# Kernel tuning notes

Measured on AMD Instinct MI355X. Metric: run time of the kernel, lower is better.

The kernel has to match this reference:

```python
import jax, jax.numpy as jnp
import numpy as np

N = 4096   # num_nodes
W = 12     # window_size
H = 256    # hidden_dim
P = 10     # prediction_horizon
E = 131072 # num edges (avg degree 32)


def setup_inputs() -> dict:
    key = jax.random.key(0)
    ks = jax.random.split(key, 12)
    return {
        "x": jax.random.normal(ks[0], (N, W), jnp.float32),
        "edge_index": jax.random.randint(ks[1], (2, E), 0, N, jnp.int32),
        "edge_weight": jax.random.uniform(ks[2], (E,), jnp.float32),
        "gcn_w": jax.random.normal(ks[3], (H,), jnp.float32) * 0.2,
        "ta_w": jax.random.normal(ks[4], (W * H, H), jnp.float32) * 0.02,
        "ta_b": jnp.zeros((H,), jnp.float32),
        "w_ih": jax.random.normal(ks[5], (3 * H, H), jnp.float32) * 0.05,
        "w_hh": jax.random.normal(ks[6], (3 * H, H), jnp.float32) * 0.05,
        "b_ih": jnp.zeros((3 * H,), jnp.float32),
        "b_hh": jnp.zeros((3 * H,), jnp.float32),
        "out_w": jax.random.normal(ks[7], (H,), jnp.float32) * 0.05,
        "out_b": jnp.zeros((1,), jnp.float32),
    }


def _laplacian(edge_index, edge_weight):
    # dense adjacency with self loops, symmetric normalization D^-1/2 (A+I)^T D^-1/2
    adj = jnp.zeros((N, N), edge_weight.dtype).at[edge_index[0], edge_index[1]].set(edge_weight)
    adj = adj + jnp.eye(N, dtype=edge_weight.dtype)
    d = jnp.power(adj.sum(1), -0.5)
    d = jnp.where(jnp.isinf(d), 0.0, d)
    # torch: adj.matmul(diag(d)).T.matmul(diag(d)) == ((adj * d[None,:]).T) * d[None,:]
    return (adj * d[None, :]).T * d[None, :]


def _gru_cell(x, h, w_ih, w_hh, b_ih, b_hh):
    gx = x @ w_ih.T + b_ih          # (N, 3H)
    gh = h @ w_hh.T + b_hh          # (N, 3H)
    xr, xz, xn = jnp.split(gx, 3, axis=-1)
    hr, hz, hn = jnp.split(gh, 3, axis=-1)
    r = jax.nn.sigmoid(xr + hr)
    z = jax.nn.sigmoid(xz + hz)
    n = jnp.tanh(xn + r * hn)
    return (1.0 - z) * n + z * h


def reference(x, edge_index, edge_weight, gcn_w, ta_w, ta_b,
              w_ih, w_hh, b_ih, b_hh, out_w, out_b):
    L = _laplacian(edge_index, edge_weight)  # fixed across all horizon steps

    def single_step(window, h):
        ax = L @ window                                   # (N, W)
        # outer product with weight vector + tanh, flattened per node
        g = jnp.tanh(ax[:, :, None] * gcn_w[None, None, :]).reshape(N, W * H)
        t = jax.nn.relu(g @ ta_w + ta_b)                  # (N, H)
        h2 = _gru_cell(t, h, w_ih, w_hh, b_ih, b_hh)      # (N, H)
        pred = h2 @ out_w + out_b[0]                      # (N,)
        return pred, h2

    def scan_step(carry, _):
        window, h = carry
        pred, h2 = single_step(window, h)
        new_window = jnp.concatenate(
            [window[:, 1:], jax.lax.stop_gradient(pred)[:, None]], axis=1)
        return (new_window, h2), pred

    h0 = jnp.zeros((N, H), x.dtype)
    _, preds = jax.lax.scan(scan_step, (x, h0), None, length=P)  # (P, N)
    return preds.T  # (N, P)
```

## Files before the change

### kernel.cpp

```cpp
#include <hip/hip_runtime.h>
#include <math.h>

#define NN 4096
#define WW 12
#define HH 256
#define PP 10
#define EE 131072
#define HS 262144
#define HMASK (HS-1)
#define TS 192
#define TA 8.0f
#define RS 22

typedef __attribute__((ext_vector_type(8))) _Float16 half8v;
typedef __attribute__((ext_vector_type(4))) _Float16 half4v;
typedef __attribute__((ext_vector_type(4))) float f32x4;

__device__ __forceinline__ float fast_tanh(float x){
  float e = __expf(2.0f*x);
  return 1.0f - 2.0f/(e+1.0f);
}
__device__ __forceinline__ float fast_sigmoid(float x){
  return 1.0f/(1.0f+__expf(-x));
}


__global__ void k_init(const float* __restrict__ x, int* keys, int* midx,
                       float* deg, int* cnt, float* ring, float* hA, int* count){
  int i = blockIdx.x*256 + threadIdx.x;
  if (i < HS){ keys[i] = -1; midx[i] = -1; }
  if (i < NN){ deg[i] = 0.0f; cnt[i] = 0; }
  if (i < NN*WW){ int n = i/WW, w = i - n*WW; ring[n*RS + w] = x[i]; }
  if (i < NN*HH) hA[i] = 0.0f;
  if (i == 0) *count = 0;
}

__global__ void k_insert(const int* __restrict__ ei, int* keys, int* midx){
  int e = blockIdx.x*256 + threadIdx.x;
  if (e >= EE) return;
  int key = ei[e]*NN + ei[EE+e];
  unsigned h = (((unsigned)key)*2654435761u >> 14) & HMASK;
  for(;;){
    int k = keys[h];
    if (k == key){ atomicMax(&midx[h], e); return; }
    if (k == -1){
      int old = atomicCAS(&keys[h], -1, key);
      if (old == -1 || old == key){ atomicMax(&midx[h], e); return; }
    }
    h = (h+1) & HMASK;
  }
}

__global__ void k_compact(const int* __restrict__ ei, const float* __restrict__ ew,
                          const int* __restrict__ keys, const int* __restrict__ midx,
                          int* wsrc, int* wdst, float* wwt,
                          float* deg, int* cnt, int* count){
  int e = blockIdx.x*256 + threadIdx.x;
  if (e >= EE) return;
  int src = ei[e], dst = ei[EE+e];
  int key = src*NN + dst;
  unsigned h = (((unsigned)key)*2654435761u >> 14) & HMASK;
  while (keys[h] != key) h = (h+1) & HMASK;
  if (midx[h] == e){
    int p = atomicAdd(count, 1);
    wsrc[p] = src; wdst[p] = dst; wwt[p] = ew[e];
    atomicAdd(&deg[src], ew[e]);
    atomicAdd(&cnt[dst], 1);
  }
}

__global__ __launch_bounds__(1024) void k_scan(const int* __restrict__ cnt,
                                               int* row_start, int* fill){
  __shared__ int sd[NN];
  int tid = threadIdx.x;
  for (int i = tid; i < NN; i += 1024) sd[i] = cnt[i];
  __syncthreads();
  for (int off = 1; off < NN; off <<= 1){
    int v[4];
    #pragma unroll
    for (int r = 0; r < 4; ++r){
      int i = tid + r*1024;
      v[r] = (i >= off) ? sd[i-off] : 0;
    }
    __syncthreads();
    #pragma unroll
    for (int r = 0; r < 4; ++r) sd[tid + r*1024] += v[r];
    __syncthreads();
  }
  for (int i = tid; i < NN; i += 1024){
    int incl = sd[i];
    row_start[i+1] = incl;
    fill[i] = incl - cnt[i];
  }
  if (tid == 0) row_start[0] = 0;
}

__global__ void k_scatter(const int* __restrict__ wsrc, const int* __restrict__ wdst,
                          const float* __restrict__ wwt, const float* __restrict__ deg,
                          int* fill, int* csr_src, float* csr_cf,
                          const int* __restrict__ count){
  int p = blockIdx.x*256 + threadIdx.x;
  if (p >= *count) return;
  int s = wsrc[p], d = wdst[p];
  float c = wwt[p] * (1.0f/sqrtf(deg[s]+1.0f)) * (1.0f/sqrtf(deg[d]+1.0f));
  int pos = atomicAdd(&fill[d], 1);
  csr_src[pos] = s;
  csr_cf[pos] = c;
}

__global__ __launch_bounds__(256) void k_tab(const float* __restrict__ gcn_w,
                                             const float* __restrict__ ta_w,
                                             float* __restrict__ tab){
  __shared__ float As[32][64];
  __shared__ float Bs[32][64];
  __shared__ float gws[256];
  int tid = threadIdx.x;
  int n0 = blockIdx.x*64;
  int m0 = blockIdx.y*64;
  int w  = blockIdx.z;
  gws[tid] = gcn_w[tid];
  __syncthreads();
  float acc[4][4] = {};
  int tm = tid >> 4, tn = tid & 15;
  const float astep = 2.0f*TA/TS;
  for (int k0 = 0; k0 < 256; k0 += 32){
    #pragma unroll
    for (int r = 0; r < 2; ++r){
      int f = tid + r*256;
      int kk = f >> 4, n4 = (f & 15)*4;
      *(float4*)&Bs[kk][n4] = *(const float4*)&ta_w[(w*256 + k0+kk)*HH + n0 + n4];
    }
    {
      int kk = tid >> 3;
      int mb = (tid & 7)*8;
      float gw = gws[k0 + kk];
      #pragma unroll
      for (int i2 = 0; i2 < 8; ++i2){
        float a = -TA + (float)(m0 + mb + i2)*astep;
        As[kk][mb+i2] = fast_tanh(a*gw);
      }
    }
    __syncthreads();
    #pragma unroll
    for (int kk = 0; kk < 32; ++kk){
      float4 a4 = *(float4*)&As[kk][tm*4];
      float4 b4 = *(float4*)&Bs[kk][tn*4];
      float a[4] = {a4.x,a4.y,a4.z,a4.w};
      float b[4] = {b4.x,b4.y,b4.z,b4.w};
      #pragma unroll
      for (int i = 0; i < 4; ++i)
        #pragma unroll
        for (int j = 0; j < 4; ++j)
          acc[i][j] = fmaf(a[i], b[j], acc[i][j]);
    }
    __syncthreads();
  }
  #pragma unroll
  for (int i = 0; i < 4; ++i){
    int row = m0 + tm*4 + i;
    if (row <= TS){
      #pragma unroll
      for (int j = 0; j < 4; ++j)
        tab[((size_t)w*(TS+1) + row)*HH + n0 + tn*4 + j] = acc[i][j];
    }
  }
}

__global__ void k_wpack(const float* __restrict__ w_ih, const float* __restrict__ w_hh,
                        _Float16* __restrict__ wp){
  int idx = blockIdx.x*256 + threadIdx.x;
  int lane = idx & 63;
  int rest = idx >> 6;
  int ct = rest & 15; rest >>= 4;
  int g  = rest & 3;
  int ks = rest >> 2;
  int col = ct*16 + (lane & 15);
  int kb  = ks*32 + (lane >> 4)*8;
  _Float16 w8[8];
  #pragma unroll
  for (int j = 0; j < 8; ++j){
    int k = kb + j;
    float v;
    if      (g == 0) v = (k < 256) ? w_ih[col*HH + k]        : w_hh[col*HH + k - 256];
    else if (g == 1) v = (k < 256) ? w_ih[(256+col)*HH + k]  : w_hh[(256+col)*HH + k - 256];
    else if (g == 2) v = (k < 256) ? w_ih[(512+col)*HH + k]  : 0.0f;
    else             v = (k < 256) ? 0.0f                    : w_hh[(512+col)*HH + k - 256];
    w8[j] = (_Float16)v;
  }
  *(half8v*)&wp[(size_t)idx*8] = *(half8v*)w8;
}

__global__ __launch_bounds__(1024, 4) void k_step(
    const int* __restrict__ rowst, const int* __restrict__ csr_src,
    const float* __restrict__ csr_cf, const float* __restrict__ deg,
    float* __restrict__ ring, const float* __restrict__ tab,
    const float* __restrict__ ta_b,
    const float* __restrict__ hc, float* __restrict__ hnb,
    const _Float16* __restrict__ wp,
    const float* __restrict__ b_ih, const float* __restrict__ b_hh,
    const float* __restrict__ out_w, const float* __restrict__ out_b,
    float* __restrict__ out, int s){

  __shared__ __align__(16) _Float16 Xh[64][17][8];
  __shared__ __align__(16) _Float16 Xl[64][17][8];
  __shared__ __align__(16) float h_pad[16][260];
  __shared__ int   sidx[16][12];
  __shared__ float sfrac[16][12];

  const int tid = threadIdx.x;
  const int n0 = blockIdx.x*16;
  const int wv = tid >> 6, lane = tid & 63;

  {
    int row = tid >> 6;
    int c0 = (tid & 63)*4;
    float4 v = *(const float4*)(hc + (size_t)(n0+row)*HH + c0);
    *(float4*)&h_pad[row][c0] = v;
    float f[4] = {v.x,v.y,v.z,v.w};
    _Float16 h4[4], l4[4];
    #pragma unroll
    for (int j = 0; j < 4; ++j){
      h4[j] = (_Float16)f[j];
      l4[j] = (_Float16)(f[j] - (float)h4[j]);
    }
    int koct = 32 + (c0 >> 3), elem = c0 & 7;
    *(half4v*)&Xh[koct][row][elem] = *(half4v*)h4;
    *(half4v*)&Xl[koct][row][elem] = *(half4v*)l4;
  }
  if (lane < 48){
    int w = lane >> 2, g = lane & 3;
    int node = n0 + wv;
    float acc0 = 0.0f;
    if (g == 0){
      float dv2 = 1.0f/(deg[node] + 1.0f);
      acc0 = dv2*ring[(size_t)node*RS + s + w];
    }
    int e1 = rowst[node+1];
    for (int e = rowst[node] + g; e < e1; e += 4)
      acc0 += csr_cf[e]*ring[(size_t)csr_src[e]*RS + s + w];
    acc0 += __shfl_xor(acc0, 1, 64);
    acc0 += __shfl_xor(acc0, 2, 64);
    if (g == 0){
      float u = (acc0 + TA) * ((float)TS/(2.0f*TA));
      u = fminf(fmaxf(u, 0.0f), (float)TS - 0.0005f);
      int i = (int)u;
      sidx[wv][w] = i;
      sfrac[wv][w] = u - (float)i;
    }
  }
  __syncthreads();

  {
    int col = tid & 255;
    int r0 = (tid >> 8)*4;
    int koct = col >> 3, elem = col & 7;
    float tb = ta_b[col];
    #pragma unroll
    for (int rr = 0; rr < 4; ++rr){
      int r = r0 + rr;
      float acc0 = tb;
      #pragma unroll
      for (int w = 0; w < 12; ++w){
        const float* pj = tab + ((size_t)w*(TS+1) + sidx[r][w])*HH + col;
        float v0 = pj[0], v1 = pj[HH];
        acc0 += v0 + sfrac[r][w]*(v1 - v0);
      }
      float tv = acc0 > 0.0f ? acc0 : 0.0f;
      _Float16 hh_ = (_Float16)tv;
      Xh[koct][r][elem] = hh_;
      Xl[koct][r][elem] = (_Float16)(tv - (float)hh_);
    }
  }
  __syncthreads();

  f32x4 acc[4];
  #pragma unroll
  for (int g = 0; g < 4; ++g) acc[g] = (f32x4){0.f,0.f,0.f,0.f};

  const int a_row = lane & 15, a_ko = lane >> 4;
  const size_t fbase = (size_t)wv*64 + lane;

  half8v b0[2], b1[2], b2[2];

#define LOADB(KS, BUF)                                                        \
  {                                                                           \
    const int G2v = ((KS) < 8) ? 2 : 3;                                       \
    const size_t fb = fbase + (size_t)(KS)*4096;                              \
    b0[BUF] = *(const half8v*)&wp[fb*8];                                      \
    b1[BUF] = *(const half8v*)&wp[(fb + 1024)*8];                             \
    b2[BUF] = *(const half8v*)&wp[(fb + (size_t)G2v*1024)*8];                 \
  }

  LOADB(0, 0)
  #pragma unroll
  for (int ks = 0; ks < 16; ++ks){
    const int cur = ks & 1, nxt = cur ^ 1;
    if (ks < 15) LOADB(ks+1, nxt)
    half8v ah = *(const half8v*)&Xh[ks*4 + a_ko][a_row][0];
    half8v al = *(const half8v*)&Xl[ks*4 + a_ko][a_row][0];
    const int G2 = (ks < 8) ? 2 : 3;
    acc[0]  = __builtin_amdgcn_mfma_f32_16x16x32_f16(ah, b0[cur], acc[0], 0,0,0);
    acc[0]  = __builtin_amdgcn_mfma_f32_16x16x32_f16(al, b0[cur], acc[0], 0,0,0);
    acc[1]  = __builtin_amdgcn_mfma_f32_16x16x32_f16(ah, b1[cur], acc[1], 0,0,0);
    acc[1]  = __builtin_amdgcn_mfma_f32_16x16x32_f16(al, b1[cur], acc[1], 0,0,0);
    acc[G2] = __builtin_amdgcn_mfma_f32_16x16x32_f16(ah, b2[cur], acc[G2], 0,0,0);
    acc[G2] = __builtin_amdgcn_mfma_f32_16x16x32_f16(al, b2[cur], acc[G2], 0,0,0);
  }
#undef LOADB
  __syncthreads();

  {
    const int ecl  = lane & 15;
    const int erow = (lane >> 4)*4;
    const int col  = wv*16 + ecl;
    float br  = b_ih[col]        + b_hh[col];
    float bz  = b_ih[col + HH]   + b_hh[col + HH];
    float bxn = b_ih[col + 2*HH];
    float bhn = b_hh[col + 2*HH];
    #pragma unroll
    for (int q = 0; q < 4; ++q){
      int row = erow + q;
      float r = fast_sigmoid(acc[0][q] + br);
      float z = fast_sigmoid(acc[1][q] + bz);
      float n = fast_tanh(acc[2][q] + bxn + r*(acc[3][q] + bhn));
      float hv = h_pad[row][col];
      float hp = (1.0f - z)*n + z*hv;
      hnb[(size_t)(n0+row)*HH + col] = hp;
      h_pad[row][col] = hp;
    }
  }
  __syncthreads();

  {
    int c0 = lane*4;
    float4 hv = *(const float4*)&h_pad[wv][c0];
    float4 w4 = *(const float4*)(out_w + c0);
    float sacc = hv.x*w4.x + hv.y*w4.y + hv.z*w4.z + hv.w*w4.w;
    sacc += __shfl_xor(sacc, 1, 64);
    sacc += __shfl_xor(sacc, 2, 64);
    sacc += __shfl_xor(sacc, 4, 64);
    sacc += __shfl_xor(sacc, 8, 64);
    sacc += __shfl_xor(sacc, 16, 64);
    sacc += __shfl_xor(sacc, 32, 64);
    if (lane == 0){
      float pv = sacc + out_b[0];
      out[(size_t)(n0+wv)*PP + s] = pv;
      ring[(size_t)(n0+wv)*RS + 12 + s] = pv;
    }
  }
}


extern "C" void kernel_launch(void* const* d_in, const int* in_sizes, int n_in,
                              void* d_out, int out_size, void* d_ws, size_t ws_size,
                              hipStream_t stream){
  const float* x     = (const float*)d_in[0];
  const int*   ei    = (const int*)  d_in[1];
  const float* ew    = (const float*)d_in[2];
  const float* gcn_w = (const float*)d_in[3];
  const float* ta_w  = (const float*)d_in[4];
  const float* ta_b  = (const float*)d_in[5];
  const float* w_ih  = (const float*)d_in[6];
  const float* w_hh  = (const float*)d_in[7];
  const float* b_ih  = (const float*)d_in[8];
  const float* b_hh  = (const float*)d_in[9];
  const float* out_w = (const float*)d_in[10];
  const float* out_b = (const float*)d_in[11];
  float* out = (float*)d_out;

  char* p = (char*)d_ws;
  float*    tab     = (float*)p;    p += (size_t)12*(TS+1)*HH*4;
  int*      keys    = (int*)p;      p += (size_t)HS*4;
  int*      midx    = (int*)p;      p += (size_t)HS*4;
  int*      wsrc    = (int*)p;      p += (size_t)EE*4;
  int*      wdst    = (int*)p;      p += (size_t)EE*4;
  float*    wwt     = (float*)p;    p += (size_t)EE*4;
  int*      csr_src = (int*)p;      p += (size_t)EE*4;
  float*    csr_cf  = (float*)p;    p += (size_t)EE*4;
  float*    deg     = (float*)p;    p += (size_t)NN*4;
  int*      cnt     = (int*)p;      p += (size_t)NN*4;
  int*      fill    = (int*)p;      p += (size_t)NN*4;
  int*      rowst   = (int*)p;      p += (size_t)(NN+64)*4;
  int*      count   = (int*)p;      p += 256;
  float*    ring    = (float*)p;    p += (size_t)NN*RS*4;
  float*    hA      = (float*)p;    p += (size_t)NN*HH*4;
  float*    hB      = (float*)p;    p += (size_t)NN*HH*4;
  _Float16* wp      = (_Float16*)p; p += (size_t)16*4*16*64*8*2;

  k_init   <<<(NN*HH)/256, 256, 0, stream>>>(x, keys, midx, deg, cnt, ring, hA, count);
  k_insert <<<EE/256, 256, 0, stream>>>(ei, keys, midx);
  k_compact<<<EE/256, 256, 0, stream>>>(ei, ew, keys, midx, wsrc, wdst, wwt, deg, cnt, count);
  k_scan   <<<1, 1024, 0, stream>>>(cnt, rowst, fill);
  k_scatter<<<EE/256, 256, 0, stream>>>(wsrc, wdst, wwt, deg, fill, csr_src, csr_cf, count);
  k_wpack  <<<256, 256, 0, stream>>>(w_ih, w_hh, wp);
  k_tab    <<<dim3(HH/64, (TS+64)/64, WW), 256, 0, stream>>>(gcn_w, ta_w, tab);

  for (int s = 0; s < PP; ++s){
    const float* hc  = (s & 1) ? hB : hA;
    float*       hnb = (s & 1) ? hA : hB;
    k_step<<<NN/16, 1024, 0, stream>>>(rowst, csr_src, csr_cf, deg, ring, tab,
                                       ta_b, hc, hnb, wp,
                                       b_ih, b_hh, out_w, out_b, out, s);
  }
}
```

Baseline: 296.2 us.

## Retile GRU step to 32 nodes x 128 columns with split-K and fp16 table

Measured after the change: 354.3 us. +19.6%, slower.

```diff
diff --git a/kernel.cpp b/kernel.cpp
--- a/kernel.cpp
+++ b/kernel.cpp
@@ -13,7 +13,6 @@
 #define RS 22
 
 typedef __attribute__((ext_vector_type(8))) _Float16 half8v;
-typedef __attribute__((ext_vector_type(4))) _Float16 half4v;
 typedef __attribute__((ext_vector_type(4))) float f32x4;
 
 __device__ __forceinline__ float fast_tanh(float x){
@@ -26,11 +25,13 @@
 
 
 __global__ void k_init(const float* __restrict__ x, int* keys, int* midx,
-                       float* deg, int* cnt, float* ring, float* hA, int* count){
+                       float* deg, int* cnt, float* ring, float* hA,
+                       float* out, int* count){
   int i = blockIdx.x*256 + threadIdx.x;
   if (i < HS){ keys[i] = -1; midx[i] = -1; }
   if (i < NN){ deg[i] = 0.0f; cnt[i] = 0; }
   if (i < NN*WW){ int n = i/WW, w = i - n*WW; ring[n*RS + w] = x[i]; }
+  if (i < NN*PP){ int n = i/PP, c = i - n*PP; ring[n*RS + 12 + c] = 0.0f; out[i] = 0.0f; }
   if (i < NN*HH) hA[i] = 0.0f;
   if (i == 0) *count = 0;
 }
@@ -110,7 +111,7 @@
 
 __global__ __launch_bounds__(256) void k_tab(const float* __restrict__ gcn_w,
                                              const float* __restrict__ ta_w,
-                                             float* __restrict__ tab){
+                                             _Float16* __restrict__ tab16){
   __shared__ float As[32][64];
   __shared__ float Bs[32][64];
   __shared__ float gws[256];
@@ -161,7 +162,7 @@
     if (row <= TS){
       #pragma unroll
       for (int j = 0; j < 4; ++j)
-        tab[((size_t)w*(TS+1) + row)*HH + n0 + tn*4 + j] = acc[i][j];
+        tab16[((size_t)w*(TS+1) + row)*HH + n0 + tn*4 + j] = (_Float16)acc[i][j];
     }
   }
 }
@@ -190,10 +191,10 @@
   *(half8v*)&wp[(size_t)idx*8] = *(half8v*)w8;
 }
 
-__global__ __launch_bounds__(1024, 4) void k_step(
+__global__ __launch_bounds__(1024) void k_step(
     const int* __restrict__ rowst, const int* __restrict__ csr_src,
     const float* __restrict__ csr_cf, const float* __restrict__ deg,
-    float* __restrict__ ring, const float* __restrict__ tab,
+    float* __restrict__ ring, const _Float16* __restrict__ tab16,
     const float* __restrict__ ta_b,
     const float* __restrict__ hc, float* __restrict__ hnb,
     const _Float16* __restrict__ wp,
@@ -201,68 +202,78 @@
     const float* __restrict__ out_w, const float* __restrict__ out_b,
     float* __restrict__ out, int s){
 
-  __shared__ __align__(16) _Float16 Xh[64][17][8];
-  __shared__ __align__(16) _Float16 Xl[64][17][8];
-  __shared__ __align__(16) float h_pad[16][260];
-  __shared__ int   sidx[16][12];
-  __shared__ float sfrac[16][12];
+  __shared__ __align__(16) _Float16 Xh[64][33][8];
+  __shared__ __align__(16) _Float16 Xl[64][33][8];
+  __shared__ __align__(16) float h_pad[32][132];
+  __shared__ float pex[8][2][64][13];
+  __shared__ int   sidx[32][12];
+  __shared__ float sfrac[32][12];
 
   const int tid = threadIdx.x;
-  const int n0 = blockIdx.x*16;
+  const int bx = blockIdx.x;
+  const int n0 = (bx >> 1)*32;
+  const int ch = bx & 1;
+  const int c0g = ch*128;
   const int wv = tid >> 6, lane = tid & 63;
+  const int ct = wv & 7, kh = wv >> 3;
 
   {
-    int row = tid >> 6;
-    int c0 = (tid & 63)*4;
-    float4 v = *(const float4*)(hc + (size_t)(n0+row)*HH + c0);
-    *(float4*)&h_pad[row][c0] = v;
-    float f[4] = {v.x,v.y,v.z,v.w};
-    _Float16 h4[4], l4[4];
-    #pragma unroll
-    for (int j = 0; j < 4; ++j){
-      h4[j] = (_Float16)f[j];
-      l4[j] = (_Float16)(f[j] - (float)h4[j]);
-    }
-    int koct = 32 + (c0 >> 3), elem = c0 & 7;
-    *(half4v*)&Xh[koct][row][elem] = *(half4v*)h4;
-    *(half4v*)&Xl[koct][row][elem] = *(half4v*)l4;
+    int row = tid >> 5;
+    int c = (tid & 31)*8;
+    const float* hr = hc + (size_t)(n0+row)*HH + c;
+    float4 v0 = *(const float4*)hr, v1 = *(const float4*)(hr+4);
+    float f[8] = {v0.x,v0.y,v0.z,v0.w,v1.x,v1.y,v1.z,v1.w};
+    _Float16 h8[8], l8[8];
+    #pragma unroll
+    for (int j = 0; j < 8; ++j){
+      h8[j] = (_Float16)f[j];
+      l8[j] = (_Float16)(f[j] - (float)h8[j]);
+    }
+    int koct = 32 + (c >> 3);
+    *(half8v*)&Xh[koct][row][0] = *(half8v*)h8;
+    *(half8v*)&Xl[koct][row][0] = *(half8v*)l8;
+    if ((c >> 7) == ch){
+      *(float4*)&h_pad[row][c & 127]       = v0;
+      *(float4*)&h_pad[row][(c & 127) + 4] = v1;
+    }
   }
   if (lane < 48){
-    int w = lane >> 2, g = lane & 3;
-    int node = n0 + wv;
+    int nl = lane/24;
+    int rem = lane - nl*24;
+    int w = rem >> 1, g = rem & 1;
+    int node = n0 + wv*2 + nl;
     float acc0 = 0.0f;
     if (g == 0){
       float dv2 = 1.0f/(deg[node] + 1.0f);
       acc0 = dv2*ring[(size_t)node*RS + s + w];
     }
     int e1 = rowst[node+1];
-    for (int e = rowst[node] + g; e < e1; e += 4)
+    for (int e = rowst[node] + g; e < e1; e += 2)
       acc0 += csr_cf[e]*ring[(size_t)csr_src[e]*RS + s + w];
     acc0 += __shfl_xor(acc0, 1, 64);
-    acc0 += __shfl_xor(acc0, 2, 64);
     if (g == 0){
       float u = (acc0 + TA) * ((float)TS/(2.0f*TA));
       u = fminf(fmaxf(u, 0.0f), (float)TS - 0.0005f);
       int i = (int)u;
-      sidx[wv][w] = i;
-      sfrac[wv][w] = u - (float)i;
+      sidx[wv*2+nl][w] = i;
+      sfrac[wv*2+nl][w] = u - (float)i;
     }
   }
   __syncthreads();
 
   {
     int col = tid & 255;
-    int r0 = (tid >> 8)*4;
+    int r0 = (tid >> 8)*8;
     int koct = col >> 3, elem = col & 7;
     float tb = ta_b[col];
     #pragma unroll
-    for (int rr = 0; rr < 4; ++rr){
+    for (int rr = 0; rr < 8; ++rr){
       int r = r0 + rr;
       float acc0 = tb;
       #pragma unroll
       for (int w = 0; w < 12; ++w){
-        const float* pj = tab + ((size_t)w*(TS+1) + sidx[r][w])*HH + col;
-        float v0 = pj[0], v1 = pj[HH];
+        const _Float16* pj = tab16 + ((size_t)w*(TS+1) + sidx[r][w])*HH + col;
+        float v0 = (float)pj[0], v1 = (float)pj[HH];
         acc0 += v0 + sfrac[r][w]*(v1 - v0);
       }
       float tv = acc0 > 0.0f ? acc0 : 0.0f;
@@ -273,79 +284,107 @@
   }
   __syncthreads();
 
-  f32x4 acc[4];
+  f32x4 acc[3][2];
   #pragma unroll
-  for (int g = 0; g < 4; ++g) acc[g] = (f32x4){0.f,0.f,0.f,0.f};
-
+  for (int g = 0; g < 3; ++g){
+    acc[g][0] = (f32x4){0.f,0.f,0.f,0.f};
+    acc[g][1] = (f32x4){0.f,0.f,0.f,0.f};
+  }
   const int a_row = lane & 15, a_ko = lane >> 4;
-  const size_t fbase = (size_t)wv*64 + lane;
-
+  const int ctg = ch*8 + ct;
+  const size_t goff2 = (size_t)(kh ? 3 : 2)*1024;
+  const size_t fb0 = (size_t)ctg*64 + lane;
   half8v b0[2], b1[2], b2[2];
 
-#define LOADB(KS, BUF)                                                        \
+#define LOADB(K8, BUF)                                                        \
   {                                                                           \
-    const int G2v = ((KS) < 8) ? 2 : 3;                                       \
-    const size_t fb = fbase + (size_t)(KS)*4096;                              \
+    const size_t fb = fb0 + (size_t)(kh*8 + (K8))*4096;                       \
     b0[BUF] = *(const half8v*)&wp[fb*8];                                      \
     b1[BUF] = *(const half8v*)&wp[(fb + 1024)*8];                             \
-    b2[BUF] = *(const half8v*)&wp[(fb + (size_t)G2v*1024)*8];                 \
+    b2[BUF] = *(const half8v*)&wp[(fb + goff2)*8];                            \
   }
 
   LOADB(0, 0)
   #pragma unroll
-  for (int ks = 0; ks < 16; ++ks){
-    const int cur = ks & 1, nxt = cur ^ 1;
-    if (ks < 15) LOADB(ks+1, nxt)
-    half8v ah = *(const half8v*)&Xh[ks*4 + a_ko][a_row][0];
-    half8v al = *(const half8v*)&Xl[ks*4 + a_ko][a_row][0];
-    const int G2 = (ks < 8) ? 2 : 3;
-    acc[0]  = __builtin_amdgcn_mfma_f32_16x16x32_f16(ah, b0[cur], acc[0], 0,0,0);
-    acc[0]  = __builtin_amdgcn_mfma_f32_16x16x32_f16(al, b0[cur], acc[0], 0,0,0);
-    acc[1]  = __builtin_amdgcn_mfma_f32_16x16x32_f16(ah, b1[cur], acc[1], 0,0,0);
-    acc[1]  = __builtin_amdgcn_mfma_f32_16x16x32_f16(al, b1[cur], acc[1], 0,0,0);
-    acc[G2] = __builtin_amdgcn_mfma_f32_16x16x32_f16(ah, b2[cur], acc[G2], 0,0,0);
-    acc[G2] = __builtin_amdgcn_mfma_f32_16x16x32_f16(al, b2[cur], acc[G2], 0,0,0);
+  for (int k8 = 0; k8 < 8; ++k8){
+    const int cur = k8 & 1, nxt = cur ^ 1;
+    if (k8 < 7) LOADB(k8+1, nxt)
+    int ko = (kh*8 + k8)*4 + a_ko;
+    half8v ah0 = *(const half8v*)&Xh[ko][a_row][0];
+    half8v al0 = *(const half8v*)&Xl[ko][a_row][0];
+    half8v ah1 = *(const half8v*)&Xh[ko][16 + a_row][0];
+    half8v al1 = *(const half8v*)&Xl[ko][16 + a_row][0];
+    acc[0][0] = __builtin_amdgcn_mfma_f32_16x16x32_f16(ah0, b0[cur], acc[0][0], 0,0,0);
+    acc[0][0] = __builtin_amdgcn_mfma_f32_16x16x32_f16(al0, b0[cur], acc[0][0], 0,0,0);
+    acc[0][1] = __builtin_amdgcn_mfma_f32_16x16x32_f16(ah1, b0[cur], acc[0][1], 0,0,0);
+    acc[0][1] = __builtin_amdgcn_mfma_f32_16x16x32_f16(al1, b0[cur], acc[0][1], 0,0,0);
+    acc[1][0] = __builtin_amdgcn_mfma_f32_16x16x32_f16(ah0, b1[cur], acc[1][0], 0,0,0);
+    acc[1][0] = __builtin_amdgcn_mfma_f32_16x16x32_f16(al0, b1[cur], acc[1][0], 0,0,0);
+    acc[1][1] = __builtin_amdgcn_mfma_f32_16x16x32_f16(ah1, b1[cur], acc[1][1], 0,0,0);
+    acc[1][1] = __builtin_amdgcn_mfma_f32_16x16x32_f16(al1, b1[cur], acc[1][1], 0,0,0);
+    acc[2][0] = __builtin_amdgcn_mfma_f32_16x16x32_f16(ah0, b2[cur], acc[2][0], 0,0,0);
+    acc[2][0] = __builtin_amdgcn_mfma_f32_16x16x32_f16(al0, b2[cur], acc[2][0], 0,0,0);
+    acc[2][1] = __builtin_amdgcn_mfma_f32_16x16x32_f16(ah1, b2[cur], acc[2][1], 0,0,0);
+    acc[2][1] = __builtin_amdgcn_mfma_f32_16x16x32_f16(al1, b2[cur], acc[2][1], 0,0,0);
   }
 #undef LOADB
   __syncthreads();
 
-  {
-    const int ecl  = lane & 15;
-    const int erow = (lane >> 4)*4;
-    const int col  = wv*16 + ecl;
+  if (kh == 0){
+    #pragma unroll
+    for (int rf = 0; rf < 2; ++rf)
+      #pragma unroll
+      for (int g3 = 0; g3 < 3; ++g3)
+        #pragma unroll
+        for (int q = 0; q < 4; ++q)
+          pex[ct][rf][lane][g3*4 + q] = acc[g3][rf][q];
+  }
+  __syncthreads();
+
+  if (kh == 1){
+    const int ecl = lane & 15;
+    const int col_l = ct*16 + ecl;
+    const int col = c0g + col_l;
     float br  = b_ih[col]        + b_hh[col];
     float bz  = b_ih[col + HH]   + b_hh[col + HH];
     float bxn = b_ih[col + 2*HH];
     float bhn = b_hh[col + 2*HH];
     #pragma unroll
-    for (int q = 0; q < 4; ++q){
-      int row = erow + q;
-      float r = fast_sigmoid(acc[0][q] + br);
-      float z = fast_sigmoid(acc[1][q] + bz);
-      float n = fast_tanh(acc[2][q] + bxn + r*(acc[3][q] + bhn));
-      float hv = h_pad[row][col];
-      float hp = (1.0f - z)*n + z*hv;
-      hnb[(size_t)(n0+row)*HH + col] = hp;
-      h_pad[row][col] = hp;
+    for (int rf = 0; rf < 2; ++rf){
+      #pragma unroll
+      for (int q = 0; q < 4; ++q){
+        int row = rf*16 + (lane >> 4)*4 + q;
+        float xr = pex[ct][rf][lane][q]     + acc[0][rf][q];
+        float xz = pex[ct][rf][lane][4 + q] + acc[1][rf][q];
+        float xn = pex[ct][rf][lane][8 + q];
+        float hn = acc[2][rf][q];
+        float r = fast_sigmoid(xr + br);
+        float z = fast_sigmoid(xz + bz);
+        float n = fast_tanh(xn + bxn + r*(hn + bhn));
+        float hv = h_pad[row][col_l];
+        float hp = (1.0f - z)*n + z*hv;
+        hnb[(size_t)(n0+row)*HH + col] = hp;
+        h_pad[row][col_l] = hp;
+      }
     }
   }
   __syncthreads();
 
   {
-    int c0 = lane*4;
-    float4 hv = *(const float4*)&h_pad[wv][c0];
-    float4 w4 = *(const float4*)(out_w + c0);
+    int row = 2*wv + (lane >> 5);
+    int cl = (lane & 31)*4;
+    float4 hv = *(const float4*)&h_pad[row][cl];
+    float4 w4 = *(const float4*)(out_w + c0g + cl);
     float sacc = hv.x*w4.x + hv.y*w4.y + hv.z*w4.z + hv.w*w4.w;
     sacc += __shfl_xor(sacc, 1, 64);
     sacc += __shfl_xor(sacc, 2, 64);
     sacc += __shfl_xor(sacc, 4, 64);
     sacc += __shfl_xor(sacc, 8, 64);
     sacc += __shfl_xor(sacc, 16, 64);
-    sacc += __shfl_xor(sacc, 32, 64);
-    if (lane == 0){
-      float pv = sacc + out_b[0];
-      out[(size_t)(n0+wv)*PP + s] = pv;
-      ring[(size_t)(n0+wv)*RS + 12 + s] = pv;
+    if ((lane & 31) == 0){
+      float part = sacc + (ch == 0 ? out_b[0] : 0.0f);
+      atomicAdd(&out[(size_t)(n0+row)*PP + s], part);
+      atomicAdd(&ring[(size_t)(n0+row)*RS + 12 + s], part);
     }
   }
 }
@@ -369,7 +408,7 @@
   float* out = (float*)d_out;
 
   char* p = (char*)d_ws;
-  float*    tab     = (float*)p;    p += (size_t)12*(TS+1)*HH*4;
+  _Float16* tab16   = (_Float16*)p; p += (size_t)12*(TS+1)*HH*2;
   int*      keys    = (int*)p;      p += (size_t)HS*4;
   int*      midx    = (int*)p;      p += (size_t)HS*4;
   int*      wsrc    = (int*)p;      p += (size_t)EE*4;
@@ -387,18 +426,18 @@
   float*    hB      = (float*)p;    p += (size_t)NN*HH*4;
   _Float16* wp      = (_Float16*)p; p += (size_t)16*4*16*64*8*2;
 
-  k_init   <<<(NN*HH)/256, 256, 0, stream>>>(x, keys, midx, deg, cnt, ring, hA, count);
+  k_init   <<<(NN*HH)/256, 256, 0, stream>>>(x, keys, midx, deg, cnt, ring, hA, out, count);
   k_insert <<<EE/256, 256, 0, stream>>>(ei, keys, midx);
   k_compact<<<EE/256, 256, 0, stream>>>(ei, ew, keys, midx, wsrc, wdst, wwt, deg, cnt, count);
   k_scan   <<<1, 1024, 0, stream>>>(cnt, rowst, fill);
   k_scatter<<<EE/256, 256, 0, stream>>>(wsrc, wdst, wwt, deg, fill, csr_src, csr_cf, count);
   k_wpack  <<<256, 256, 0, stream>>>(w_ih, w_hh, wp);
-  k_tab    <<<dim3(HH/64, (TS+64)/64, WW), 256, 0, stream>>>(gcn_w, ta_w, tab);
+  k_tab    <<<dim3(HH/64, (TS+64)/64, WW), 256, 0, stream>>>(gcn_w, ta_w, tab16);
 
   for (int s = 0; s < PP; ++s){
     const float* hc  = (s & 1) ? hB : hA;
     float*       hnb = (s & 1) ? hA : hB;
-    k_step<<<NN/16, 1024, 0, stream>>>(rowst, csr_src, csr_cf, deg, ring, tab,
+    k_step<<<NN/16, 1024, 0, stream>>>(rowst, csr_src, csr_cf, deg, ring, tab16,
                                        ta_b, hc, hnb, wp,
                                        b_ih, b_hh, out_w, out_b, out, s);
   }
```
